# Performance work log

Hardware: AMD Instinct MI355X
Metric: run time of the kernel (lower is better)

## Reference

```python
import jax, jax.numpy as jnp
import numpy as np

B = 512          # batch
V = 6890         # SMPL vertices
NB = 10          # num_betas
NJ = 24          # joints (root + 23 body)
# canonical SMPL kinematic tree (parents[0] = -1 for root)
PARENTS = np.array([-1,0,0,0,1,2,3,4,5,6,7,8,9,9,9,12,13,14,16,17,18,19,20,21], dtype=np.int32)


def rodrigues(rot_vecs):
    """Axis-angle [N,3] -> rotation matrices [N,3,3] (matches batch_rodrigues)."""
    angle = jnp.linalg.norm(rot_vecs + 1e-8, axis=1, keepdims=True)  # [N,1]
    rot_dir = rot_vecs / angle
    cos = jnp.cos(angle)[:, :, None]  # [N,1,1]
    sin = jnp.sin(angle)[:, :, None]
    rx, ry, rz = rot_dir[:, 0], rot_dir[:, 1], rot_dir[:, 2]
    zeros = jnp.zeros_like(rx)
    K = jnp.stack([zeros, -rz, ry,
                   rz, zeros, -rx,
                   -ry, rx, zeros], axis=1).reshape(-1, 3, 3)
    I = jnp.eye(3, dtype=rot_vecs.dtype)
    return I[None] + sin * K + (1.0 - cos) * jnp.matmul(K, K)


def setup_inputs() -> dict:
    key = jax.random.key(0)
    ks = jax.random.split(key, 8)
    betas = jnp.concatenate([jnp.ones((B, 1), jnp.float32),
                             0.5 * jax.random.normal(ks[0], (B, NB), jnp.float32)], axis=1)
    body_pose = 0.3 * jax.random.normal(ks[1], (B, 3 * (NJ - 1)), jnp.float32)
    global_orient = 0.3 * jax.random.normal(ks[2], (B, 3), jnp.float32)
    transl = jax.random.normal(ks[3], (B, 3), jnp.float32)
    shapedirs = 0.01 * jax.random.normal(ks[4], (V, 3, NB), jnp.float32)
    v_template = jax.random.normal(ks[5], (V, 3), jnp.float32)
    Jr = jax.random.uniform(ks[6], (NJ, V), jnp.float32)
    Jr = Jr / jnp.sum(Jr, axis=1, keepdims=True)
    W = jax.random.uniform(ks[7], (V, NJ), jnp.float32)
    W = W / jnp.sum(W, axis=1, keepdims=True)             # convex skinning weights
    return dict(betas=betas, body_pose=body_pose, global_orient=global_orient,
                transl=transl, shapedirs=shapedirs, v_template=v_template,
                J_regressor=Jr, lbs_weights=W)


def reference(betas, body_pose, global_orient, transl,
              shapedirs, v_template, J_regressor, lbs_weights):
    dt = v_template.dtype
    blend = jnp.einsum('bl,mkl->bmk', betas[:, 1:], shapedirs)            # [B,V,3]
    v_shaped = (v_template[None] + blend) * betas[:, 0][:, None, None]    # [B,V,3]
    J = jnp.einsum('bik,ji->bjk', v_shaped, J_regressor)                  # [B,NJ,3]
    # ---- updatePose: axis-angle -> rotmats
    full_pose = jnp.concatenate([global_orient, body_pose], axis=1)       # [B,NJ*3]
    rot_mats = rodrigues(full_pose.reshape(-1, 3)).reshape(-1, NJ, 3, 3)  # [B,NJ,3,3]
    # ---- kinematic chain (batch_rigid_transform)
    rel = J.at[:, 1:].add(-J[:, PARENTS[1:]])                             # rel joint offsets
    T_local = jnp.concatenate([rot_mats, rel[..., None]], axis=3)         # [B,NJ,3,4]
    bottom = jnp.broadcast_to(jnp.array([0, 0, 0, 1], dt), (rot_mats.shape[0], NJ, 1, 4))
    T_local = jnp.concatenate([T_local, bottom], axis=2)                  # [B,NJ,4,4]
    chain = [T_local[:, 0]]
    for i in range(1, NJ):  # fixed 24-node tree
        chain.append(jnp.matmul(chain[PARENTS[i]], T_local[:, i]))
    transforms = jnp.stack(chain, axis=1)                                 # [B,NJ,4,4]
    J_transformed = transforms[:, :, :3, 3]                               # [B,NJ,3]
    # relative transforms: subtract rotated rest joint from translation column
    init_t = jnp.einsum('bnij,bnj->bni', transforms[:, :, :3, :3], J)
    A = transforms.at[:, :, :3, 3].add(-init_t)                           # [B,NJ,4,4]
    # ---- skinning: T = W @ A, apply to homogeneous verts
    T = jnp.einsum('vn,bnij->bvij', lbs_weights, A)                       # [B,V,4,4]
    verts = (jnp.einsum('bvij,bvj->bvi', T[:, :, :3, :3], v_shaped)
             + T[:, :, :3, 3] + transl[:, None])                          # [B,V,3]
    return verts, J_transformed
```

## Files before the change

### kernel.cpp

```cpp
#include <hip/hip_runtime.h>

#define BATCH 512
#define V 6890
#define NJ 24
#define VH (V/2)

#define SD_N (V*30)
#define VT_N (V*3)
#define W_N  (V*24)
#define TOT_PK (SD_N+VT_N+W_N)
#define PREP_BLOCKS ((TOT_PK+255)/256)

#define A_OFF   0
#define BS_OFF  147456
#define JT_OFF  155648
#define JS_OFF  155720
#define PK_OFF  156672

__device__ const int d_par[NJ] = {-1,0,0,0,1,2,3,4,5,6,7,8,9,9,9,12,13,14,16,17,18,19,20,21};

__global__ __launch_bounds__(256) void prepjreg_k(
    const float* __restrict__ sd, const float* __restrict__ vt, const float* __restrict__ W,
    const float* __restrict__ Jr,
    float* __restrict__ dst, float* __restrict__ JTo, float* __restrict__ JSo)
{
  __shared__ float red[4*33];
  const int bid = blockIdx.x;
  if (bid < PREP_BLOCKS){
    int i = bid*256 + threadIdx.x;
    if (i >= TOT_PK) return;
    float val;
    if (i < SD_N){ int j=i/V, v=i-j*V; val = sd[v*30+j]; }
    else if (i < SD_N+VT_N){ int o=i-SD_N; int j=o/V, v=o-j*V; val = vt[v*3+j]; }
    else { int o=i-SD_N-VT_N; int j=o/V, v=o-j*V; val = W[v*24+j]; }
    dst[i] = val;
    return;
  }
  const int j = bid - PREP_BLOCKS;
  const int t = threadIdx.x;
  float acc[33];
#pragma unroll
  for (int m=0;m<33;m++) acc[m]=0.f;
  for (int v=t; v<V; v+=256){
    const float jr = Jr[j*V+v];
    const float* __restrict__ vp = vt + v*3;
    acc[0] = fmaf(jr, vp[0], acc[0]);
    acc[1] = fmaf(jr, vp[1], acc[1]);
    acc[2] = fmaf(jr, vp[2], acc[2]);
    const float2* __restrict__ sp = (const float2*)(sd + v*30);
#pragma unroll
    for (int m=0;m<15;m++){
      const float2 s = sp[m];
      acc[3+2*m]   = fmaf(jr, s.x, acc[3+2*m]);
      acc[3+2*m+1] = fmaf(jr, s.y, acc[3+2*m+1]);
    }
  }
  const int lane = t & 63, wid = t >> 6;
#pragma unroll
  for (int m=0;m<33;m++){
    float x = acc[m];
    x += __shfl_xor(x, 1);
    x += __shfl_xor(x, 2);
    x += __shfl_xor(x, 4);
    x += __shfl_xor(x, 8);
    x += __shfl_xor(x, 16);
    x += __shfl_xor(x, 32);
    if (lane == 0) red[wid*33+m] = x;
  }
  __syncthreads();
  if (t < 33){
    const float s = red[t] + red[33+t] + red[66+t] + red[99+t];
    if (t < 3) JTo[j*3+t] = s;
    else       JSo[j*30 + (t-3)] = s;
  }
}

__global__ __launch_bounds__(64) void batch_k(
    const float* __restrict__ betas, const float* __restrict__ body_pose,
    const float* __restrict__ go, const float* __restrict__ transl,
    const float* __restrict__ JT, const float* __restrict__ JS,
    float* __restrict__ A, float* __restrict__ bsc, float* __restrict__ jout)
{
  const int b = blockIdx.x;
  const int t = threadIdx.x;
  __shared__ float lb[11];
  __shared__ float lJ[72];
  __shared__ float lR[NJ*9];
  __shared__ float lL[NJ*12];
  __shared__ float lW[NJ*12];
  if (t < 11) lb[t] = betas[b*11+t];
  __syncthreads();
  const float b0 = lb[0];
  for (int idx=t; idx<72; idx+=64){
    float s = JT[idx];
    #pragma unroll
    for (int l=0;l<10;l++) s = fmaf(lb[1+l], JS[idx*10+l], s);
    lJ[idx] = b0*s;
  }
  if (t==0) bsc[b*16] = b0;
  if (t>=1 && t<11) bsc[b*16+t] = b0*lb[t];
  if (t<3) bsc[b*16+11+t] = transl[b*3+t];
  if (t < NJ){
    float p0,p1,p2;
    if (t==0){ p0=go[b*3+0]; p1=go[b*3+1]; p2=go[b*3+2]; }
    else { int o=b*69+(t-1)*3; p0=body_pose[o]; p1=body_pose[o+1]; p2=body_pose[o+2]; }
    float a0=p0+1e-8f, a1=p1+1e-8f, a2=p2+1e-8f;
    float angle = sqrtf(a0*a0+a1*a1+a2*a2);
    float inv = 1.0f/angle;
    float rx=p0*inv, ry=p1*inv, rz=p2*inv;
    float sn = sinf(angle), cs = cosf(angle), mc = 1.0f-cs;
    float K[9] = {0.f,-rz,ry, rz,0.f,-rx, -ry,rx,0.f};
    float KK[9];
    #pragma unroll
    for (int r=0;r<3;r++)
      #pragma unroll
      for (int c=0;c<3;c++)
        KK[r*3+c] = K[r*3+0]*K[0+c] + K[r*3+1]*K[3+c] + K[r*3+2]*K[6+c];
    #pragma unroll
    for (int e=0;e<9;e++){
      float ident = (e==0||e==4||e==8)?1.0f:0.0f;
      lR[t*9+e] = ident + sn*K[e] + mc*KK[e];
    }
  }
  __syncthreads();
  for (int idx=t; idx<288; idx+=64){
    int j = idx/12, rc = idx-12*j, r = rc>>2, c = rc&3;
    float val;
    if (c<3) val = lR[j*9 + r*3 + c];
    else {
      int p = (j==0) ? 0 : d_par[j];
      val = (j==0) ? lJ[r] : (lJ[j*3+r] - lJ[p*3+r]);
    }
    lL[idx] = val;
  }
  __syncthreads();
  if (t<12) lW[t] = lL[t];
  __syncthreads();
  for (int i=1;i<NJ;i++){
    if (t<12){
      int p = d_par[i];
      int r = t>>2, c = t&3;
      float s = lW[p*12+r*4+0]*lL[i*12+0+c]
              + lW[p*12+r*4+1]*lL[i*12+4+c]
              + lW[p*12+r*4+2]*lL[i*12+8+c];
      if (c==3) s += lW[p*12+r*4+3];
      lW[i*12+t] = s;
    }
    __syncthreads();
  }
  for (int idx=t; idx<72; idx+=64){
    int j=idx/3, k=idx-3*j;
    jout[b*72+idx] = lW[j*12+k*4+3];
  }
  const int g = b>>1, q = b&1;
  float* __restrict__ Ab = A + g*576 + q*12;
  for (int idx=t; idx<288; idx+=64){
    int n=idx/12, rc=idx-12*n, r=rc>>2, c=rc&3;
    float val = lW[n*12+rc];
    if (c==3){
      val -= lW[n*12+r*4+0]*lJ[n*3+0] + lW[n*12+r*4+1]*lJ[n*3+1] + lW[n*12+r*4+2]*lJ[n*3+2];
    }
    Ab[n*24 + rc] = val;
  }
}

__global__ __launch_bounds__(256, 8) void main_k(
    const float* __restrict__ A, const float* __restrict__ bsc,
    const float2* __restrict__ pk, float* __restrict__ out)
{
  const int vh = blockIdx.x*256 + threadIdx.x;
  if (vh >= VH) return;
  const int bg = blockIdx.y;
  const float* __restrict__ Ag = A + bg*576;
  const float* __restrict__ bs = bsc + bg*32;

  const float2 vt0 = pk[30*VH + vh];
  const float2 vt1 = pk[31*VH + vh];
  const float2 vt2 = pk[32*VH + vh];

  float2 vs[2][3];
#pragma unroll
  for (int q=0;q<2;q++){
    const float b0 = bs[q*16];
    vs[q][0] = make_float2(b0*vt0.x, b0*vt0.y);
    vs[q][1] = make_float2(b0*vt1.x, b0*vt1.y);
    vs[q][2] = make_float2(b0*vt2.x, b0*vt2.y);
  }
#pragma unroll
  for (int l=0;l<10;l++){
    const float2 s0 = pk[(0*10+l)*VH + vh];
    const float2 s1 = pk[(1*10+l)*VH + vh];
    const float2 s2 = pk[(2*10+l)*VH + vh];
#pragma unroll
    for (int q=0;q<2;q++){
      const float c = bs[q*16+1+l];
      vs[q][0].x = fmaf(c, s0.x, vs[q][0].x); vs[q][0].y = fmaf(c, s0.y, vs[q][0].y);
      vs[q][1].x = fmaf(c, s1.x, vs[q][1].x); vs[q][1].y = fmaf(c, s1.y, vs[q][1].y);
      vs[q][2].x = fmaf(c, s2.x, vs[q][2].x); vs[q][2].y = fmaf(c, s2.y, vs[q][2].y);
    }
  }

  float y[2][6];
#pragma unroll
  for (int q=0;q<2;q++)
#pragma unroll
    for (int i=0;i<6;i++) y[q][i] = 0.f;

#pragma unroll 4
  for (int n=0;n<NJ;n++){
    const float2 w = pk[(33+n)*VH + vh];
#pragma unroll
    for (int q=0;q<2;q++){
      const float* __restrict__ an = Ag + n*24 + q*12;
      float tt;
      tt = fmaf(an[2], vs[q][2].x, fmaf(an[1], vs[q][1].x, fmaf(an[0], vs[q][0].x, an[3])));
      y[q][0] = fmaf(w.x, tt, y[q][0]);
      tt = fmaf(an[2], vs[q][2].y, fmaf(an[1], vs[q][1].y, fmaf(an[0], vs[q][0].y, an[3])));
      y[q][1] = fmaf(w.y, tt, y[q][1]);
      tt = fmaf(an[6], vs[q][2].x, fmaf(an[5], vs[q][1].x, fmaf(an[4], vs[q][0].x, an[7])));
      y[q][2] = fmaf(w.x, tt, y[q][2]);
      tt = fmaf(an[6], vs[q][2].y, fmaf(an[5], vs[q][1].y, fmaf(an[4], vs[q][0].y, an[7])));
      y[q][3] = fmaf(w.y, tt, y[q][3]);
      tt = fmaf(an[10], vs[q][2].x, fmaf(an[9], vs[q][1].x, fmaf(an[8], vs[q][0].x, an[11])));
      y[q][4] = fmaf(w.x, tt, y[q][4]);
      tt = fmaf(an[10], vs[q][2].y, fmaf(an[9], vs[q][1].y, fmaf(an[8], vs[q][0].y, an[11])));
      y[q][5] = fmaf(w.y, tt, y[q][5]);
    }
  }

  const int v0 = 2*vh;
#pragma unroll
  for (int q=0;q<2;q++){
    const float t0 = bs[q*16+11], t1 = bs[q*16+12], t2 = bs[q*16+13];
    const int b = bg*2 + q;
    float2* __restrict__ o2 = (float2*)(out + (b*V + v0)*3);
    o2[0] = make_float2(y[q][0]+t0, y[q][2]+t1);
    o2[1] = make_float2(y[q][4]+t2, y[q][1]+t0);
    o2[2] = make_float2(y[q][3]+t1, y[q][5]+t2);
  }
}

extern "C" void kernel_launch(void* const* d_in, const int* in_sizes, int n_in,
                              void* d_out, int out_size, void* d_ws, size_t ws_size,
                              hipStream_t stream)
{
  const float* betas     = (const float*)d_in[0];
  const float* body_pose = (const float*)d_in[1];
  const float* go        = (const float*)d_in[2];
  const float* transl    = (const float*)d_in[3];
  const float* sdirs     = (const float*)d_in[4];
  const float* vtempl    = (const float*)d_in[5];
  const float* Jr        = (const float*)d_in[6];
  const float* lw        = (const float*)d_in[7];
  float* wsf = (float*)d_ws;
  float* out = (float*)d_out;

  hipLaunchKernelGGL(prepjreg_k, dim3(PREP_BLOCKS + 24), dim3(256), 0, stream,
                     sdirs, vtempl, lw, Jr, wsf+PK_OFF, wsf+JT_OFF, wsf+JS_OFF);
  hipLaunchKernelGGL(batch_k, dim3(BATCH), dim3(64), 0, stream,
                     betas, body_pose, go, transl, wsf+JT_OFF, wsf+JS_OFF,
                     wsf+A_OFF, wsf+BS_OFF, out + BATCH*V*3);
  hipLaunchKernelGGL(main_k, dim3((VH+255)/256, BATCH/2), dim3(256), 0, stream,
                     wsf+A_OFF, wsf+BS_OFF, (const float2*)(wsf+PK_OFF), out);
}
```

Before: 149.9 us.

## Fuse per-batch kinematic chain into skinning kernel and split joint regression

Removes the separate per-batch transform kernel and recomputes each batch pair's joint transforms inside every skinning block. The kinematic chain is evaluated with wavefront shuffles over tree depth, and the result is kept in shared memory instead of a global workspace. Joint regression is split across 8 vertex chunks per joint, combined with atomics after a memset. This drops one launch and the global round trip of A, at the cost of redundant chain computation in every vertex block, plus the extra memset and atomic traffic.

```diff
diff --git a/kernel.cpp b/kernel.cpp
--- a/kernel.cpp
+++ b/kernel.cpp
@@ -10,14 +10,16 @@
 #define W_N  (V*24)
 #define TOT_PK (SD_N+VT_N+W_N)
 #define PREP_BLOCKS ((TOT_PK+255)/256)
-
-#define A_OFF   0
-#define BS_OFF  147456
+#define NCH 8
+#define JREG_BLOCKS (NJ*NCH)
+#define CH_SZ ((V+NCH-1)/NCH)
+
 #define JT_OFF  155648
 #define JS_OFF  155720
 #define PK_OFF  156672
 
 __device__ const int d_par[NJ] = {-1,0,0,0,1,2,3,4,5,6,7,8,9,9,9,12,13,14,16,17,18,19,20,21};
+__device__ const int d_dep[NJ] = {0,1,1,1,2,2,2,3,3,3,4,4,4,4,4,5,5,5,6,6,7,7,8,8};
 
 __global__ __launch_bounds__(256) void prepjreg_k(
     const float* __restrict__ sd, const float* __restrict__ vt, const float* __restrict__ W,
@@ -26,8 +28,9 @@
 {
   __shared__ float red[4*33];
   const int bid = blockIdx.x;
+  const int t = threadIdx.x;
   if (bid < PREP_BLOCKS){
-    int i = bid*256 + threadIdx.x;
+    int i = bid*256 + t;
     if (i >= TOT_PK) return;
     float val;
     if (i < SD_N){ int j=i/V, v=i-j*V; val = sd[v*30+j]; }
@@ -36,12 +39,15 @@
     dst[i] = val;
     return;
   }
-  const int j = bid - PREP_BLOCKS;
-  const int t = threadIdx.x;
+  const int r  = bid - PREP_BLOCKS;
+  const int j  = r % NJ;
+  const int ch = r / NJ;
+  const int v0 = ch*CH_SZ;
+  const int v1 = (v0+CH_SZ < V) ? v0+CH_SZ : V;
   float acc[33];
 #pragma unroll
   for (int m=0;m<33;m++) acc[m]=0.f;
-  for (int v=t; v<V; v+=256){
+  for (int v=v0+t; v<v1; v+=256){
     const float jr = Jr[j*V+v];
     const float* __restrict__ vp = vt + v*3;
     acc[0] = fmaf(jr, vp[0], acc[0]);
@@ -70,135 +76,148 @@
   __syncthreads();
   if (t < 33){
     const float s = red[t] + red[33+t] + red[66+t] + red[99+t];
-    if (t < 3) JTo[j*3+t] = s;
-    else       JSo[j*30 + (t-3)] = s;
+    if (t < 3) atomicAdd(&JTo[j*3+t], s);
+    else       atomicAdd(&JSo[j*30 + (t-3)], s);
   }
 }
 
-__global__ __launch_bounds__(64) void batch_k(
+__global__ __launch_bounds__(256, 8) void fused_k(
     const float* __restrict__ betas, const float* __restrict__ body_pose,
     const float* __restrict__ go, const float* __restrict__ transl,
     const float* __restrict__ JT, const float* __restrict__ JS,
-    float* __restrict__ A, float* __restrict__ bsc, float* __restrict__ jout)
+    const float2* __restrict__ pk, float* __restrict__ out, float* __restrict__ jout)
 {
-  const int b = blockIdx.x;
   const int t = threadIdx.x;
-  __shared__ float lb[11];
-  __shared__ float lJ[72];
-  __shared__ float lR[NJ*9];
-  __shared__ float lL[NJ*12];
-  __shared__ float lW[NJ*12];
-  if (t < 11) lb[t] = betas[b*11+t];
+  const int vh = blockIdx.x*256 + t;
+  const bool valid = (vh < VH);
+  const int bg = blockIdx.y;
+  __shared__ float lA[NJ*24];
+
+  float b0s[2], cf[2][10], tr[2][3];
+#pragma unroll
+  for (int q=0;q<2;q++){
+    const float* __restrict__ bp = betas + (bg*2+q)*11;
+    const float bb0 = bp[0];
+    b0s[q] = bb0;
+#pragma unroll
+    for (int l=0;l<10;l++) cf[q][l] = bb0*bp[1+l];
+    const float* __restrict__ tp = transl + (bg*2+q)*3;
+    tr[q][0]=tp[0]; tr[q][1]=tp[1]; tr[q][2]=tp[2];
+  }
+
+  if (t < 56){
+    const int q = t >> 5, j = t & 31;
+    if (j < NJ){
+      const int b = bg*2 + q;
+      const float* __restrict__ bp = betas + b*11;
+      float be[11];
+#pragma unroll
+      for (int i=0;i<11;i++) be[i] = bp[i];
+      float Jv[3];
+#pragma unroll
+      for (int k=0;k<3;k++){
+        float s = JT[j*3+k];
+#pragma unroll
+        for (int l=0;l<10;l++) s = fmaf(be[1+l], JS[j*30 + k*10 + l], s);
+        Jv[k] = be[0]*s;
+      }
+      float p0,p1,p2;
+      if (j==0){ p0=go[b*3+0]; p1=go[b*3+1]; p2=go[b*3+2]; }
+      else { int o=b*69+(j-1)*3; p0=body_pose[o]; p1=body_pose[o+1]; p2=body_pose[o+2]; }
+      float a0=p0+1e-8f, a1=p1+1e-8f, a2=p2+1e-8f;
+      float angle = sqrtf(a0*a0+a1*a1+a2*a2);
+      float inv = 1.0f/angle;
+      float rx=p0*inv, ry=p1*inv, rz=p2*inv;
+      float sn = sinf(angle), cs = cosf(angle), mc = 1.0f-cs;
+      float K[9] = {0.f,-rz,ry, rz,0.f,-rx, -ry,rx,0.f};
+      float KK[9];
+#pragma unroll
+      for (int rr=0;rr<3;rr++)
+#pragma unroll
+        for (int cc=0;cc<3;cc++)
+          KK[rr*3+cc] = K[rr*3+0]*K[0+cc] + K[rr*3+1]*K[3+cc] + K[rr*3+2]*K[6+cc];
+      float R[9];
+#pragma unroll
+      for (int e=0;e<9;e++){
+        float ident = (e==0||e==4||e==8)?1.0f:0.0f;
+        R[e] = ident + sn*K[e] + mc*KK[e];
+      }
+      const int par = d_par[j];
+      const int dep = d_dep[j];
+      const int parlane = ((j==0)?0:par) + (q<<5);
+      const float Jp0 = __shfl(Jv[0], parlane);
+      const float Jp1 = __shfl(Jv[1], parlane);
+      const float Jp2 = __shfl(Jv[2], parlane);
+      float l[12];
+      l[0]=R[0]; l[1]=R[1]; l[2]=R[2];  l[3]  = (j==0)? Jv[0] : Jv[0]-Jp0;
+      l[4]=R[3]; l[5]=R[4]; l[6]=R[5];  l[7]  = (j==0)? Jv[1] : Jv[1]-Jp1;
+      l[8]=R[6]; l[9]=R[7]; l[10]=R[8]; l[11] = (j==0)? Jv[2] : Jv[2]-Jp2;
+      float w[12];
+#pragma unroll
+      for (int k=0;k<12;k++) w[k] = l[k];
+#pragma unroll
+      for (int d=1; d<=8; d++){
+        float wp[12];
+#pragma unroll
+        for (int k=0;k<12;k++) wp[k] = __shfl(w[k], parlane);
+        float c[12];
+#pragma unroll
+        for (int rr=0;rr<3;rr++){
+#pragma unroll
+          for (int cc=0;cc<4;cc++){
+            float s = wp[rr*4+0]*l[0*4+cc] + wp[rr*4+1]*l[1*4+cc] + wp[rr*4+2]*l[2*4+cc];
+            if (cc==3) s += wp[rr*4+3];
+            c[rr*4+cc] = s;
+          }
+        }
+        const bool sel = (dep == d);
+#pragma unroll
+        for (int k=0;k<12;k++) w[k] = sel ? c[k] : w[k];
+      }
+      if (blockIdx.x == 0){
+        float* __restrict__ jo = jout + b*72 + j*3;
+        jo[0]=w[3]; jo[1]=w[7]; jo[2]=w[11];
+      }
+      w[3]  -= w[0]*Jv[0] + w[1]*Jv[1] + w[2]*Jv[2];
+      w[7]  -= w[4]*Jv[0] + w[5]*Jv[1] + w[6]*Jv[2];
+      w[11] -= w[8]*Jv[0] + w[9]*Jv[1] + w[10]*Jv[2];
+      const int base = j*24 + q*12;
+      *(float4*)&lA[base+0] = make_float4(w[0],w[1],w[2],w[3]);
+      *(float4*)&lA[base+4] = make_float4(w[4],w[5],w[6],w[7]);
+      *(float4*)&lA[base+8] = make_float4(w[8],w[9],w[10],w[11]);
+    }
+  }
+
+  float2 vs[2][3];
+  if (valid){
+    const float2 vt0 = pk[30*VH + vh];
+    const float2 vt1 = pk[31*VH + vh];
+    const float2 vt2 = pk[32*VH + vh];
+#pragma unroll
+    for (int q=0;q<2;q++){
+      const float b0 = b0s[q];
+      vs[q][0] = make_float2(b0*vt0.x, b0*vt0.y);
+      vs[q][1] = make_float2(b0*vt1.x, b0*vt1.y);
+      vs[q][2] = make_float2(b0*vt2.x, b0*vt2.y);
+    }
+#pragma unroll
+    for (int l=0;l<10;l++){
+      const float2 s0 = pk[(0*10+l)*VH + vh];
+      const float2 s1 = pk[(1*10+l)*VH + vh];
+      const float2 s2 = pk[(2*10+l)*VH + vh];
+#pragma unroll
+      for (int q=0;q<2;q++){
+        const float c = cf[q][l];
+        vs[q][0].x = fmaf(c, s0.x, vs[q][0].x); vs[q][0].y = fmaf(c, s0.y, vs[q][0].y);
+        vs[q][1].x = fmaf(c, s1.x, vs[q][1].x); vs[q][1].y = fmaf(c, s1.y, vs[q][1].y);
+        vs[q][2].x = fmaf(c, s2.x, vs[q][2].x); vs[q][2].y = fmaf(c, s2.y, vs[q][2].y);
+      }
+    }
+  }
+
   __syncthreads();
-  const float b0 = lb[0];
-  for (int idx=t; idx<72; idx+=64){
-    float s = JT[idx];
-    #pragma unroll
-    for (int l=0;l<10;l++) s = fmaf(lb[1+l], JS[idx*10+l], s);
-    lJ[idx] = b0*s;
-  }
-  if (t==0) bsc[b*16] = b0;
-  if (t>=1 && t<11) bsc[b*16+t] = b0*lb[t];
-  if (t<3) bsc[b*16+11+t] = transl[b*3+t];
-  if (t < NJ){
-    float p0,p1,p2;
-    if (t==0){ p0=go[b*3+0]; p1=go[b*3+1]; p2=go[b*3+2]; }
-    else { int o=b*69+(t-1)*3; p0=body_pose[o]; p1=body_pose[o+1]; p2=body_pose[o+2]; }
-    float a0=p0+1e-8f, a1=p1+1e-8f, a2=p2+1e-8f;
-    float angle = sqrtf(a0*a0+a1*a1+a2*a2);
-    float inv = 1.0f/angle;
-    float rx=p0*inv, ry=p1*inv, rz=p2*inv;
-    float sn = sinf(angle), cs = cosf(angle), mc = 1.0f-cs;
-    float K[9] = {0.f,-rz,ry, rz,0.f,-rx, -ry,rx,0.f};
-    float KK[9];
-    #pragma unroll
-    for (int r=0;r<3;r++)
-      #pragma unroll
-      for (int c=0;c<3;c++)
-        KK[r*3+c] = K[r*3+0]*K[0+c] + K[r*3+1]*K[3+c] + K[r*3+2]*K[6+c];
-    #pragma unroll
-    for (int e=0;e<9;e++){
-      float ident = (e==0||e==4||e==8)?1.0f:0.0f;
-      lR[t*9+e] = ident + sn*K[e] + mc*KK[e];
-    }
-  }
-  __syncthreads();
-  for (int idx=t; idx<288; idx+=64){
-    int j = idx/12, rc = idx-12*j, r = rc>>2, c = rc&3;
-    float val;
-    if (c<3) val = lR[j*9 + r*3 + c];
-    else {
-      int p = (j==0) ? 0 : d_par[j];
-      val = (j==0) ? lJ[r] : (lJ[j*3+r] - lJ[p*3+r]);
-    }
-    lL[idx] = val;
-  }
-  __syncthreads();
-  if (t<12) lW[t] = lL[t];
-  __syncthreads();
-  for (int i=1;i<NJ;i++){
-    if (t<12){
-      int p = d_par[i];
-      int r = t>>2, c = t&3;
-      float s = lW[p*12+r*4+0]*lL[i*12+0+c]
-              + lW[p*12+r*4+1]*lL[i*12+4+c]
-              + lW[p*12+r*4+2]*lL[i*12+8+c];
-      if (c==3) s += lW[p*12+r*4+3];
-      lW[i*12+t] = s;
-    }
-    __syncthreads();
-  }
-  for (int idx=t; idx<72; idx+=64){
-    int j=idx/3, k=idx-3*j;
-    jout[b*72+idx] = lW[j*12+k*4+3];
-  }
-  const int g = b>>1, q = b&1;
-  float* __restrict__ Ab = A + g*576 + q*12;
-  for (int idx=t; idx<288; idx+=64){
-    int n=idx/12, rc=idx-12*n, r=rc>>2, c=rc&3;
-    float val = lW[n*12+rc];
-    if (c==3){
-      val -= lW[n*12+r*4+0]*lJ[n*3+0] + lW[n*12+r*4+1]*lJ[n*3+1] + lW[n*12+r*4+2]*lJ[n*3+2];
-    }
-    Ab[n*24 + rc] = val;
-  }
-}
-
-__global__ __launch_bounds__(256, 8) void main_k(
-    const float* __restrict__ A, const float* __restrict__ bsc,
-    const float2* __restrict__ pk, float* __restrict__ out)
-{
-  const int vh = blockIdx.x*256 + threadIdx.x;
-  if (vh >= VH) return;
-  const int bg = blockIdx.y;
-  const float* __restrict__ Ag = A + bg*576;
-  const float* __restrict__ bs = bsc + bg*32;
-
-  const float2 vt0 = pk[30*VH + vh];
-  const float2 vt1 = pk[31*VH + vh];
-  const float2 vt2 = pk[32*VH + vh];
-
-  float2 vs[2][3];
-#pragma unroll
-  for (int q=0;q<2;q++){
-    const float b0 = bs[q*16];
-    vs[q][0] = make_float2(b0*vt0.x, b0*vt0.y);
-    vs[q][1] = make_float2(b0*vt1.x, b0*vt1.y);
-    vs[q][2] = make_float2(b0*vt2.x, b0*vt2.y);
-  }
-#pragma unroll
-  for (int l=0;l<10;l++){
-    const float2 s0 = pk[(0*10+l)*VH + vh];
-    const float2 s1 = pk[(1*10+l)*VH + vh];
-    const float2 s2 = pk[(2*10+l)*VH + vh];
-#pragma unroll
-    for (int q=0;q<2;q++){
-      const float c = bs[q*16+1+l];
-      vs[q][0].x = fmaf(c, s0.x, vs[q][0].x); vs[q][0].y = fmaf(c, s0.y, vs[q][0].y);
-      vs[q][1].x = fmaf(c, s1.x, vs[q][1].x); vs[q][1].y = fmaf(c, s1.y, vs[q][1].y);
-      vs[q][2].x = fmaf(c, s2.x, vs[q][2].x); vs[q][2].y = fmaf(c, s2.y, vs[q][2].y);
-    }
-  }
+
+  if (!valid) return;
 
   float y[2][6];
 #pragma unroll
@@ -211,19 +230,21 @@
     const float2 w = pk[(33+n)*VH + vh];
 #pragma unroll
     for (int q=0;q<2;q++){
-      const float* __restrict__ an = Ag + n*24 + q*12;
+      const float4 A0 = *(const float4*)&lA[n*24+q*12+0];
+      const float4 A1 = *(const float4*)&lA[n*24+q*12+4];
+      const float4 A2 = *(const float4*)&lA[n*24+q*12+8];
       float tt;
-      tt = fmaf(an[2], vs[q][2].x, fmaf(an[1], vs[q][1].x, fmaf(an[0], vs[q][0].x, an[3])));
+      tt = fmaf(A0.z, vs[q][2].x, fmaf(A0.y, vs[q][1].x, fmaf(A0.x, vs[q][0].x, A0.w)));
       y[q][0] = fmaf(w.x, tt, y[q][0]);
-      tt = fmaf(an[2], vs[q][2].y, fmaf(an[1], vs[q][1].y, fmaf(an[0], vs[q][0].y, an[3])));
+      tt = fmaf(A0.z, vs[q][2].y, fmaf(A0.y, vs[q][1].y, fmaf(A0.x, vs[q][0].y, A0.w)));
       y[q][1] = fmaf(w.y, tt, y[q][1]);
-      tt = fmaf(an[6], vs[q][2].x, fmaf(an[5], vs[q][1].x, fmaf(an[4], vs[q][0].x, an[7])));
+      tt = fmaf(A1.z, vs[q][2].x, fmaf(A1.y, vs[q][1].x, fmaf(A1.x, vs[q][0].x, A1.w)));
       y[q][2] = fmaf(w.x, tt, y[q][2]);
-      tt = fmaf(an[6], vs[q][2].y, fmaf(an[5], vs[q][1].y, fmaf(an[4], vs[q][0].y, an[7])));
+      tt = fmaf(A1.z, vs[q][2].y, fmaf(A1.y, vs[q][1].y, fmaf(A1.x, vs[q][0].y, A1.w)));
       y[q][3] = fmaf(w.y, tt, y[q][3]);
-      tt = fmaf(an[10], vs[q][2].x, fmaf(an[9], vs[q][1].x, fmaf(an[8], vs[q][0].x, an[11])));
+      tt = fmaf(A2.z, vs[q][2].x, fmaf(A2.y, vs[q][1].x, fmaf(A2.x, vs[q][0].x, A2.w)));
       y[q][4] = fmaf(w.x, tt, y[q][4]);
-      tt = fmaf(an[10], vs[q][2].y, fmaf(an[9], vs[q][1].y, fmaf(an[8], vs[q][0].y, an[11])));
+      tt = fmaf(A2.z, vs[q][2].y, fmaf(A2.y, vs[q][1].y, fmaf(A2.x, vs[q][0].y, A2.w)));
       y[q][5] = fmaf(w.y, tt, y[q][5]);
     }
   }
@@ -231,7 +252,7 @@
   const int v0 = 2*vh;
 #pragma unroll
   for (int q=0;q<2;q++){
-    const float t0 = bs[q*16+11], t1 = bs[q*16+12], t2 = bs[q*16+13];
+    const float t0 = tr[q][0], t1 = tr[q][1], t2 = tr[q][2];
     const int b = bg*2 + q;
     float2* __restrict__ o2 = (float2*)(out + (b*V + v0)*3);
     o2[0] = make_float2(y[q][0]+t0, y[q][2]+t1);
@@ -255,11 +276,10 @@
   float* wsf = (float*)d_ws;
   float* out = (float*)d_out;
 
-  hipLaunchKernelGGL(prepjreg_k, dim3(PREP_BLOCKS + 24), dim3(256), 0, stream,
+  hipMemsetAsync((void*)(wsf+JT_OFF), 0, 792*sizeof(float), stream);
+  hipLaunchKernelGGL(prepjreg_k, dim3(PREP_BLOCKS + JREG_BLOCKS), dim3(256), 0, stream,
                      sdirs, vtempl, lw, Jr, wsf+PK_OFF, wsf+JT_OFF, wsf+JS_OFF);
-  hipLaunchKernelGGL(batch_k, dim3(BATCH), dim3(64), 0, stream,
+  hipLaunchKernelGGL(fused_k, dim3((VH+255)/256, BATCH/2), dim3(256), 0, stream,
                      betas, body_pose, go, transl, wsf+JT_OFF, wsf+JS_OFF,
-                     wsf+A_OFF, wsf+BS_OFF, out + BATCH*V*3);
-  hipLaunchKernelGGL(main_k, dim3((VH+255)/256, BATCH/2), dim3(256), 0, stream,
-                     wsf+A_OFF, wsf+BS_OFF, (const float2*)(wsf+PK_OFF), out);
+                     (const float2*)(wsf+PK_OFF), out, out + BATCH*V*3);
 }
```

Measured after the change: 353.0 us. 136% more time.
